# Kernel optimization log

Hardware: AMD Instinct MI355X
Metric: run time of the kernel (lower is better)

The kernel has to match this reference:

```python
import jax, jax.numpy as jnp
import numpy as np

K = 3
STRIDE = 1
PAD = 1
DIL = 1


def _conv2d(x, w, b, stride, pad):
    y = jax.lax.conv_general_dilated(
        x, w, (stride, stride), [(pad, pad), (pad, pad)],
        dimension_numbers=('NCHW', 'OIHW', 'NCHW'))
    return y + b[None, :, None, None]


def setup_inputs() -> dict:
    key = jax.random.key(0)
    ks = jax.random.split(key, 6)
    N, Cin, Cout, H, W = 4, 64, 64, 128, 128
    x = jax.random.normal(ks[0], (N, Cin, H, W), jnp.float32)
    w_off = jax.random.normal(ks[1], (2 * K * K, Cin, K, K), jnp.float32) * 0.01
    b_off = jnp.zeros((2 * K * K,), jnp.float32)
    w_mask = jax.random.normal(ks[2], (K * K, Cin, K, K), jnp.float32) * 0.01
    b_mask = jnp.zeros((K * K,), jnp.float32)
    weight = jax.random.normal(ks[3], (Cout, Cin, K, K), jnp.float32) * 0.05
    bias = jax.random.normal(ks[4], (Cout,), jnp.float32)
    return {"x": x, "w_off": w_off, "b_off": b_off,
            "w_mask": w_mask, "b_mask": b_mask,
            "weight": weight, "bias": bias}


def _deform_conv(x, offset, weight, bias):
    # x: [N,C,H,W]; offset: [N,2*K2,Ho,Wo] with channel layout (dy,dx) per kernel pt
    N, C, H, W = x.shape
    K2 = K * K
    Ho, Wo = offset.shape[2], offset.shape[3]
    off_y = offset[:, 0::2]  # [N,K2,Ho,Wo]
    off_x = offset[:, 1::2]
    ki = jnp.arange(K2) // K
    kj = jnp.arange(K2) % K
    base_y = (jnp.arange(Ho) * STRIDE - PAD)[None, :, None] + (ki * DIL)[:, None, None]
    base_x = (jnp.arange(Wo) * STRIDE - PAD)[None, None, :] + (kj * DIL)[:, None, None]
    py = base_y[None].astype(off_y.dtype) + off_y  # [N,K2,Ho,Wo]
    px = base_x[None].astype(off_x.dtype) + off_x
    y0 = jnp.floor(py)
    x0 = jnp.floor(px)
    wy = py - y0
    wx = px - x0
    xf = x.reshape(N, C, H * W)

    def corner(yi, xi):
        valid = (yi >= 0) & (yi <= H - 1) & (xi >= 0) & (xi <= W - 1)
        yc = jnp.clip(yi, 0, H - 1).astype(jnp.int32)
        xc = jnp.clip(xi, 0, W - 1).astype(jnp.int32)
        idx = (yc * W + xc).reshape(N, -1)  # [N, K2*Ho*Wo]
        g = jnp.take_along_axis(xf, idx[:, None, :], axis=2)  # [N,C,K2*Ho*Wo]
        g = g.reshape(N, C, K2, Ho, Wo)
        return g * valid[:, None].astype(x.dtype)

    # bilinear interpolation with zero padding outside the image
    val = ((1 - wy) * (1 - wx))[:, None] * corner(y0, x0) \
        + ((1 - wy) * wx)[:, None] * corner(y0, x0 + 1) \
        + (wy * (1 - wx))[:, None] * corner(y0 + 1, x0) \
        + (wy * wx)[:, None] * corner(y0 + 1, x0 + 1)  # [N,C,K2,Ho,Wo]
    out = jnp.einsum('nckhw,ock->nohw', val,
                     weight.reshape(weight.shape[0], C, K2))
    return out + bias[None, :, None, None]


def reference(x, w_off, b_off, w_mask, b_mask, weight, bias):
    offset = _conv2d(x, w_off, b_off, STRIDE, PAD)              # [N,2*K2,Ho,Wo]
    mask = jax.nn.sigmoid(_conv2d(x, w_mask, b_mask, STRIDE, PAD))  # [N,K2,Ho,Wo]
    # source does mask.repeat(1,2,1,1) then offset*mask, then plain deform_conv2d
    offset = offset * jnp.concatenate([mask, mask], axis=1)
    return _deform_conv(x, offset, weight, bias)
```

## Files before the change

### kernel.cpp

```cpp
#include <hip/hip_runtime.h>
#include <math.h>

#define HD 128
#define WD 128
#define WP 130
#define CIN 64
#define COUT 64
#define NB 4
#define K2 9
#define HW (HD*WD)
#define CK 576
#define TP 32
#define TPF 16
#define NKK 18

#define WAM   (4 * NKK * 64 * 8)
#define WAO   (2 * NKK * 64 * 8)
#define XTP   ((size_t)NB * WP * WP * CIN)
#define OFFSZ ((size_t)NB * K2 * HW)
#define WTSZ  ((size_t)CK * COUT)

#define PRE_T 1024
#define PRE_H 65
#define PRE_P ((WAM + WAO) / 256)
#define HALO_PER_N 33024
#define HALO_W8 16512

typedef __attribute__((ext_vector_type(8))) short short8;
typedef __attribute__((ext_vector_type(4))) float f32x4;

__device__ inline unsigned short f2bf(float v) {
    unsigned int u = __float_as_uint(v);
    unsigned int r = u + 0x7fffu + ((u >> 16) & 1u);
    return (unsigned short)(r >> 16);
}
__device__ inline float bf2f(unsigned short b) {
    return __uint_as_float(((unsigned int)b) << 16);
}
__device__ inline unsigned int pack_bf16(float a, float b) {
#if __has_builtin(__builtin_amdgcn_cvt_pk_bf16_f32)
    auto r = __builtin_amdgcn_cvt_pk_bf16_f32(a, b);
    unsigned int u; __builtin_memcpy(&u, &r, 4); return u;
#else
    return ((unsigned int)f2bf(b) << 16) | (unsigned int)f2bf(a);
#endif
}
__device__ inline float2 up2(unsigned int u) {
    float2 r;
    r.x = __uint_as_float(u << 16);
    r.y = __uint_as_float(u & 0xffff0000u);
    return r;
}

__global__ __launch_bounds__(256) void pre_kernel(
    const float* __restrict__ x,
    const float* __restrict__ weight,
    const float* __restrict__ w_off,
    const float* __restrict__ w_mask,
    unsigned short* __restrict__ xp,
    short* __restrict__ mhi, short* __restrict__ ohi)
{
    __shared__ float tile[64][66];
    int bid = blockIdx.x;
    int t = threadIdx.x;

    if (bid < PRE_T) {
        int half = bid & 1;
        int h = (bid >> 1) & 127;
        int n = bid >> 8;
        int w0 = half * 64;
        int g = t >> 6, wl = t & 63;
        const float* xb = x + ((size_t)n * CIN) * HW + h * WD + w0;
        #pragma unroll
        for (int i = 0; i < 16; i++) {
            int cc = i * 4 + g;
            tile[wl][cc] = xb[(size_t)cc * HW + wl];
        }
        __syncthreads();
        size_t rowbase = (((size_t)n * WP + (h + 1)) * WP + (w0 + 1)) * CIN;
        #pragma unroll
        for (int i = 0; i < 8; i++) {
            int u = i * 256 + t;
            int ww = u >> 5;
            int cp = (u & 31) * 2;
            float2 v = *(const float2*)&tile[ww][cp];
            *(unsigned int*)&xp[rowbase + (size_t)ww * CIN + cp] = pack_bf16(v.x, v.y);
        }
    } else if (bid < PRE_T + PRE_H) {
        int widx = (bid - PRE_T) * 256 + t;
        if (widx < HALO_W8) {
            int s = widx * 8;
            int n = s / HALO_PER_N;
            int v = s - n * HALO_PER_N;
            size_t nb = (size_t)n * WP * WP * CIN;
            size_t base;
            if (v < 8320) {
                base = nb + v;
            } else if (v < 16640) {
                base = nb + (size_t)129 * WP * CIN + (v - 8320);
            } else if (v < 24832) {
                int v2 = v - 16640; int h = 1 + (v2 >> 6); int c = v2 & 63;
                base = nb + (size_t)h * WP * CIN + c;
            } else {
                int v3 = v - 24832; int h = 1 + (v3 >> 6); int c = v3 & 63;
                base = nb + ((size_t)h * WP + 129) * CIN + c;
            }
            short8 z = {0, 0, 0, 0, 0, 0, 0, 0};
            *(short8*)&xp[base] = z;
        }
    } else {
        int gid = (bid - PRE_T - PRE_H) * 256 + t;
        if (gid < WAM) {
            int idx = gid;
            int jj = idx & 7;
            int lane = (idx >> 3) & 63;
            int kk = (idx >> 9) % NKK;
            int mt = (idx >> 9) / NKK;
            int o = mt * 16 + (lane & 15);
            int rp = kk * 32 + (lane >> 4) * 8 + jj;
            int k = rp >> 6, c = rp & 63;
            mhi[idx] = (short)f2bf(weight[((size_t)o * CIN + c) * 9 + k]);
        } else {
            int idx = gid - WAM;
            int jj = idx & 7;
            int lane = (idx >> 3) & 63;
            int kk = (idx >> 9) % NKK;
            int mt = (idx >> 9) / NKK;
            int j = mt * 16 + (lane & 15);
            int rp = kk * 32 + (lane >> 4) * 8 + jj;
            int k = rp >> 6, c = rp & 63;
            float w = 0.f;
            if (j < 18)      w = w_off[((size_t)j * CIN + c) * 9 + k];
            else if (j < 27) w = w_mask[((size_t)(j - 18) * CIN + c) * 9 + k];
            ohi[idx] = (short)f2bf(w);
        }
    }
}

__global__ __launch_bounds__(256, 4) void fused_kernel(
    const unsigned short* __restrict__ xp,
    const short* __restrict__ waM_hi,
    const short* __restrict__ waO_hi,
    const float* __restrict__ b_off, const float* __restrict__ b_mask,
    const float* __restrict__ bias,
    float* __restrict__ out)
{
    __shared__ __align__(16) short val_s[72 * 256];
    __shared__ __align__(16) float U[27 * 32];

    int t = threadIdx.x;
    int wv = t >> 6;
    int lane = t & 63;
    int wo0 = blockIdx.x * TP;
    int ho  = blockIdx.y;
    int n   = blockIdx.z;
    const unsigned short* xpn = xp + (size_t)n * WP * WP * CIN;
    int p16 = lane & 15, quad = lane >> 4;

    #pragma unroll
    for (int i = 0; i < 9; i++) {
        int u = t + 256 * i;
        int tap = u >> 8;
        int p = (u >> 3) & 31;
        int g = u & 7;
        int ti = tap / 3, tj = tap - ti * 3;
        const short8 v = *(const short8*)&xpn[((size_t)(ho + ti) * WP + (wo0 + p + tj)) * CIN + g * 8];
        int c2 = tap * 8 + g;
        *(short8*)&val_s[c2 * 256 + ((p + c2) & 31) * 8] = v;
    }
    __syncthreads();

    {
        int jt = wv >> 1, pt = wv & 1;
        f32x4 acc = {0.f, 0.f, 0.f, 0.f};
        #pragma unroll
        for (int kk = 0; kk < NKK; kk++) {
            int abase = ((jt * NKK + kk) * 64 + lane) * 8;
            short8 ah = *(const short8*)&waO_hi[abase];
            int c2 = kk * 4 + quad;
            short8 b = *(const short8*)&val_s[c2 * 256 + ((pt * 16 + p16 + c2) & 31) * 8];
            acc = __builtin_amdgcn_mfma_f32_16x16x32_bf16(ah, b, acc, 0, 0, 0);
        }
        #pragma unroll
        for (int i = 0; i < 4; i++) {
            int j = jt * 16 + quad * 4 + i;
            if (j < 27) {
                float bv = (j < 18) ? b_off[j] : b_mask[j - 18];
                U[j * 32 + pt * 16 + p16] = acc[i] + bv;
            }
        }
    }
    __syncthreads();

    float rwy[2], rwx[2];
    unsigned int rmeta[2];
    #pragma unroll
    for (int pass = 0; pass < 2; pass++) {
        int u = t + pass * 256;
        if (u < K2 * TP) {
            int k = u >> 5, p = u & 31;
            float oy_raw = U[(2 * k) * 32 + p];
            float ox_raw = U[(2 * k + 1) * 32 + p];
            float my = 1.f / (1.f + expf(-U[(18 + (2 * k) % 9) * 32 + p]));
            float mx = 1.f / (1.f + expf(-U[(18 + (2 * k + 1) % 9) * 32 + p]));
            float oy = oy_raw * my;
            float ox = ox_raw * mx;
            int ki = k / 3, kj = k - ki * 3;
            int wo = wo0 + p;
            float py = (float)(ho - 1 + ki) + oy;
            float px = (float)(wo - 1 + kj) + ox;
            float y0f = floorf(py), x0f = floorf(px);
            float wy = py - y0f, wx = px - x0f;
            int y0 = (int)y0f, x0 = (int)x0f;
            int y0c = min(max(y0, 0), HD - 1);
            int y1c = min(max(y0 + 1, 0), HD - 1);
            int x0c = min(max(x0, 0), WD - 1);
            int x1c = min(max(x0 + 1, 0), WD - 1);
            bool vy0 = (y0 >= 0) && (y0 < HD);
            bool vy1 = (y0 + 1 >= 0) && (y0 + 1 < HD);
            bool vx0 = (x0 >= 0) && (x0 < WD);
            bool vx1 = (x0 + 1 >= 0) && (x0 + 1 < WD);
            unsigned int cvA = (vy0 && vx0) ? 1u : 0u;
            unsigned int cvB = (vy0 && vx1) ? 1u : 0u;
            unsigned int cvC = (vy1 && vx0) ? 1u : 0u;
            unsigned int cvD = (vy1 && vx1) ? 1u : 0u;
            rwy[pass] = wy;
            rwx[pass] = wx;
            rmeta[pass] = (unsigned int)y0c | ((unsigned int)x0c << 7)
                        | ((unsigned int)(y1c - y0c) << 14) | ((unsigned int)(x1c - x0c) << 15)
                        | (cvA << 16) | (cvB << 17) | (cvC << 18) | (cvD << 19);
        }
    }
    __syncthreads();
    #pragma unroll
    for (int pass = 0; pass < 2; pass++) {
        int u = t + pass * 256;
        if (u < K2 * TP) {
            U[u] = rwy[pass];
            U[288 + u] = rwx[pass];
            ((unsigned int*)U)[576 + u] = rmeta[pass];
        }
    }
    __syncthreads();

    #pragma unroll
    for (int i = 0; i < 9; i++) {
        int u = t + 256 * i;
        int task = u >> 3;
        int g = u & 7;
        int c0 = g * 8;
        int k = task >> 5, p = task & 31;
        float wy = U[task];
        float wx = U[288 + task];
        unsigned int m = ((const unsigned int*)U)[576 + task];
        float wy0 = 1.f - wy, wx0 = 1.f - wx;
        float wA = (m & 0x10000u) ? wy0 * wx0 : 0.f;
        float wB = (m & 0x20000u) ? wy0 * wx  : 0.f;
        float wC = (m & 0x40000u) ? wy  * wx0 : 0.f;
        float wD = (m & 0x80000u) ? wy  * wx  : 0.f;
        int y0c = (int)(m & 127u);
        int x0c = (int)((m >> 7) & 127u);
        int ry0 = (y0c + 1) * (WP * CIN);
        int ry1 = ry0 + (int)((m >> 14) & 1u) * (WP * CIN);
        int cx0 = (x0c + 1) * CIN;
        int cx1 = cx0 + (int)((m >> 15) & 1u) * CIN;
        int ia = ry0 + cx0 + c0;
        int ib = ry0 + cx1 + c0;
        int ic = ry1 + cx0 + c0;
        int id = ry1 + cx1 + c0;
        uint4 qa = *(const uint4*)&xpn[ia];
        uint4 qb = *(const uint4*)&xpn[ib];
        uint4 qc = *(const uint4*)&xpn[ic];
        uint4 qd = *(const uint4*)&xpn[id];
        unsigned int qa_[4] = {qa.x, qa.y, qa.z, qa.w};
        unsigned int qb_[4] = {qb.x, qb.y, qb.z, qb.w};
        unsigned int qc_[4] = {qc.x, qc.y, qc.z, qc.w};
        unsigned int qd_[4] = {qd.x, qd.y, qd.z, qd.w};
        unsigned int r_[4];
        #pragma unroll
        for (int d = 0; d < 4; d++) {
            float2 fa = up2(qa_[d]), fb = up2(qb_[d]), fc = up2(qc_[d]), fd = up2(qd_[d]);
            float2 gg;
            gg.x = wA * fa.x + wB * fb.x + wC * fc.x + wD * fd.x;
            gg.y = wA * fa.y + wB * fb.y + wC * fc.y + wD * fd.y;
            r_[d] = pack_bf16(gg.x, gg.y);
        }
        uint4 r = {r_[0], r_[1], r_[2], r_[3]};
        int c2 = k * 8 + g;
        *(uint4*)&val_s[c2 * 256 + ((p + c2) & 31) * 8] = r;
    }
    __syncthreads();

    f32x4 a0 = {0.f, 0.f, 0.f, 0.f};
    f32x4 a1 = {0.f, 0.f, 0.f, 0.f};
    #pragma unroll
    for (int kk = 0; kk < NKK; kk++) {
        int abase = ((wv * NKK + kk) * 64 + lane) * 8;
        short8 ah = *(const short8*)&waM_hi[abase];
        int c2 = kk * 4 + quad;
        short8 b0 = *(const short8*)&val_s[c2 * 256 + ((p16 + c2) & 31) * 8];
        short8 b1 = *(const short8*)&val_s[c2 * 256 + ((16 + p16 + c2) & 31) * 8];
        a0 = __builtin_amdgcn_mfma_f32_16x16x32_bf16(ah, b0, a0, 0, 0, 0);
        a1 = __builtin_amdgcn_mfma_f32_16x16x32_bf16(ah, b1, a1, 0, 0, 0);
    }

    size_t obase = ((size_t)n * COUT) * HW + (size_t)ho * WD + wo0;
    #pragma unroll
    for (int i = 0; i < 4; i++) {
        int o = wv * 16 + quad * 4 + i;
        float bv = bias[o];
        out[obase + (size_t)o * HW + p16] = a0[i] + bv;
        out[obase + (size_t)o * HW + 16 + p16] = a1[i] + bv;
    }
}

__global__ void transpose_w_kernel(const float* __restrict__ w, float* __restrict__ wt) {
    int i = blockIdx.x * 256 + threadIdx.x;
    int o = i / CK;
    int ck = i - o * CK;
    wt[ck * COUT + o] = w[i];
}

__global__ __launch_bounds__(256) void offmask_kernel(
    const float* __restrict__ x,
    const float* __restrict__ w_off, const float* __restrict__ b_off,
    const float* __restrict__ w_mask, const float* __restrict__ b_mask,
    float* __restrict__ offy, float* __restrict__ offx)
{
    __shared__ float ws[CK][27];
    int t = threadIdx.x;
    for (int i = t; i < CK * 27; i += 256) {
        int j = i % 27;
        int citap = i / 27;
        int ci = citap / 9;
        int tap = citap - ci * 9;
        float v;
        if (j < 18) v = w_off[(j * CIN + ci) * 9 + tap];
        else        v = w_mask[((j - 18) * CIN + ci) * 9 + tap];
        ws[citap][j] = v;
    }
    __syncthreads();

    int pix = blockIdx.x * 256 + t;
    int n  = pix >> 14;
    int ho = (pix >> 7) & 127;
    int wo = pix & 127;

    float acc[27];
    #pragma unroll
    for (int j = 0; j < 18; j++) acc[j] = b_off[j];
    #pragma unroll
    for (int j = 0; j < 9; j++)  acc[18 + j] = b_mask[j];

    int offs[9];
    bool oks[9];
    #pragma unroll
    for (int dy = 0; dy < 3; dy++) {
        int y = ho - 1 + dy;
        #pragma unroll
        for (int dx = 0; dx < 3; dx++) {
            int xx = wo - 1 + dx;
            bool ok = (y >= 0) && (y < HD) && (xx >= 0) && (xx < WD);
            oks[dy * 3 + dx] = ok;
            offs[dy * 3 + dx] = (ok ? y : 0) * WD + (ok ? xx : 0);
        }
    }
    const float* xn = x + (size_t)n * CIN * HW;
    for (int ci = 0; ci < CIN; ci++) {
        const float* xc = xn + (size_t)ci * HW;
        float v[9];
        #pragma unroll
        for (int tap = 0; tap < 9; tap++)
            v[tap] = oks[tap] ? xc[offs[tap]] : 0.f;
        #pragma unroll
        for (int tap = 0; tap < 9; tap++) {
            const float* wrow = ws[ci * 9 + tap];
            float vv = v[tap];
            #pragma unroll
            for (int j = 0; j < 27; j++) acc[j] += wrow[j] * vv;
        }
    }
    float m[9];
    #pragma unroll
    for (int j = 0; j < 9; j++) m[j] = 1.f / (1.f + expf(-acc[18 + j]));
    #pragma unroll
    for (int k = 0; k < 9; k++) {
        int cy = 2 * k, cx = 2 * k + 1;
        float my = m[cy < 9 ? cy : cy - 9];
        float mx = m[cx < 9 ? cx : cx - 9];
        size_t o = (((size_t)n * K2 + k) * HD + ho) * WD + wo;
        offy[o] = acc[cy] * my;
        offx[o] = acc[cx] * mx;
    }
}

__global__ __launch_bounds__(256) void deform_kernel(
    const float* __restrict__ x,
    const float* __restrict__ offy, const float* __restrict__ offx,
    const float* __restrict__ wt,
    const float* __restrict__ bias,
    float* __restrict__ out)
{
    __shared__ __align__(16) float val_f[CK * TPF];
    __shared__ float4 p_w4[K2 * TPF];
    __shared__ int4   p_idx4[K2 * TPF];

    int t = threadIdx.x;
    int wo0 = blockIdx.x * TPF;
    int ho  = blockIdx.y;
    int n   = blockIdx.z;

    if (t < K2 * TPF) {
        int k = t >> 4, p = t & 15;
        int wo = wo0 + p;
        size_t oi = (((size_t)n * K2 + k) * HD + ho) * WD + wo;
        float oy = offy[oi], ox = offx[oi];
        int ki = k / 3, kj = k - ki * 3;
        float py = (float)(ho - 1 + ki) + oy;
        float px = (float)(wo - 1 + kj) + ox;
        float y0f = floorf(py), x0f = floorf(px);
        float wy = py - y0f, wx = px - x0f;
        int y0 = (int)y0f, x0 = (int)x0f;
        float wy0 = 1.f - wy, wx0 = 1.f - wx;
        int y0c = min(max(y0, 0), HD - 1);
        int y1c = min(max(y0 + 1, 0), HD - 1);
        int x0c = min(max(x0, 0), WD - 1);
        int x1c = min(max(x0 + 1, 0), WD - 1);
        bool vy0 = (y0 >= 0) && (y0 < HD);
        bool vy1 = (y0 + 1 >= 0) && (y0 + 1 < HD);
        bool vx0 = (x0 >= 0) && (x0 < WD);
        bool vx1 = (x0 + 1 >= 0) && (x0 + 1 < WD);
        float4 w4;
        w4.x = (vy0 && vx0) ? wy0 * wx0 : 0.f;
        w4.y = (vy0 && vx1) ? wy0 * wx  : 0.f;
        w4.z = (vy1 && vx0) ? wy  * wx0 : 0.f;
        w4.w = (vy1 && vx1) ? wy  * wx  : 0.f;
        int4 i4;
        i4.x = y0c * WD + x0c;
        i4.y = y0c * WD + x1c;
        i4.z = y1c * WD + x0c;
        i4.w = y1c * WD + x1c;
        p_w4[t] = w4;
        p_idx4[t] = i4;
    }
    __syncthreads();

    const float* xn = x + (size_t)n * CIN * HW;
    for (int e = t; e < CK * TPF; e += 256) {
        int row = e >> 4, p = e & 15;
        int cc = row / 9, k = row - cc * 9;
        int task = (k << 4) | p;
        float4 w4 = p_w4[task];
        int4  i4 = p_idx4[task];
        const float* xc = xn + (size_t)cc * HW;
        val_f[e] = w4.x * xc[i4.x] + w4.y * xc[i4.y]
                 + w4.z * xc[i4.z] + w4.w * xc[i4.w];
    }
    __syncthreads();

    int o = t & 63, q = t >> 6;
    float4 acc = {0.f, 0.f, 0.f, 0.f};
    const float4* v4 = (const float4*)val_f;
    const float* wp = wt + o;
    #pragma unroll 4
    for (int r = 0; r < CK; r++) {
        float w = wp[r * COUT];
        float4 vv = v4[r * 4 + q];
        acc.x += w * vv.x; acc.y += w * vv.y;
        acc.z += w * vv.z; acc.w += w * vv.w;
    }
    float b = bias[o];
    acc.x += b; acc.y += b; acc.z += b; acc.w += b;
    __syncthreads();
    float4* o4 = (float4*)val_f;
    o4[o * 4 + q] = acc;
    __syncthreads();
    size_t obase = ((size_t)n * COUT) * HW + (size_t)ho * WD + wo0;
    #pragma unroll
    for (int i = 0; i < 4; i++) {
        int l = t + 256 * i;
        int oo = l >> 4, p = l & 15;
        out[obase + (size_t)oo * HW + p] = val_f[l];
    }
}

extern "C" void kernel_launch(void* const* d_in, const int* in_sizes, int n_in,
                              void* d_out, int out_size, void* d_ws, size_t ws_size,
                              hipStream_t stream) {
    const float* x      = (const float*)d_in[0];
    const float* w_off  = (const float*)d_in[1];
    const float* b_off  = (const float*)d_in[2];
    const float* w_mask = (const float*)d_in[3];
    const float* b_mask = (const float*)d_in[4];
    const float* weight = (const float*)d_in[5];
    const float* bias   = (const float*)d_in[6];
    float* out = (float*)d_out;

    short* base = (short*)d_ws;
    short* waM_hi = base;
    short* waO_hi = waM_hi + WAM;
    unsigned short* xp = (unsigned short*)(waO_hi + WAO);
    size_t need = ((size_t)WAM + WAO + XTP) * sizeof(short);

    if (ws_size >= need) {
        pre_kernel<<<PRE_T + PRE_H + PRE_P, 256, 0, stream>>>(
            x, weight, w_off, w_mask, xp, waM_hi, waO_hi);
        fused_kernel<<<dim3(WD / TP, HD, NB), 256, 0, stream>>>(
            xp, waM_hi, waO_hi, b_off, b_mask, bias, out);
    } else {
        float* offy = (float*)d_ws;
        float* offx = offy + OFFSZ;
        float* wt   = offx + OFFSZ;
        transpose_w_kernel<<<144, 256, 0, stream>>>(weight, wt);
        offmask_kernel<<<256, 256, 0, stream>>>(x, w_off, b_off, w_mask, b_mask, offy, offx);
        deform_kernel<<<dim3(WD / TPF, HD, NB), 256, 0, stream>>>(x, offy, offx, wt, bias, out);
    }
}
```

Before: 111.3 us.

## Fuse offset setup into bilinear sampling with software-pipelined corner gathers

Drops the separate pass that computed per-tap bilinear metadata into shared memory, along with its two barriers. Each thread now handles one pixel and channel group across all 9 taps, computing the 9 sigmoid masks once and prefetching corner loads two taps ahead in a 3-slot register ring. The im2col staging loop is also restructured so all 9 global loads are issued before the shared stores. The cost is redundant offset math (each of the 8 channel-group threads recomputes it) and higher register pressure, which could hurt occupancy under launch_bounds(256,4).

```diff
diff --git a/kernel.cpp b/kernel.cpp
--- a/kernel.cpp
+++ b/kernel.cpp
@@ -137,6 +137,37 @@
     }
 }
 
+#define TAP_SETUP(kc, s) { \
+    const int kk_ = (kc); \
+    float oy = U[(2 * kk_) * 32 + p] * msk[(2 * kk_) % 9]; \
+    float ox = U[(2 * kk_ + 1) * 32 + p] * msk[(2 * kk_ + 1) % 9]; \
+    const int ki_ = kk_ / 3, kj_ = kk_ - ki_ * 3; \
+    float py = (float)(ho - 1 + ki_) + oy; \
+    float px = (float)(wo0 + p - 1 + kj_) + ox; \
+    float y0f = floorf(py), x0f = floorf(px); \
+    float wy = py - y0f, wx = px - x0f; \
+    int y0 = (int)y0f, x0 = (int)x0f; \
+    int y0c = min(max(y0, 0), HD - 1); \
+    int y1c = min(max(y0 + 1, 0), HD - 1); \
+    int x0c = min(max(x0, 0), WD - 1); \
+    int x1c = min(max(x0 + 1, 0), WD - 1); \
+    bool vy0 = (y0 >= 0) && (y0 < HD); \
+    bool vy1 = (y0 + 1 >= 0) && (y0 + 1 < HD); \
+    bool vx0 = (x0 >= 0) && (x0 < WD); \
+    bool vx1 = (x0 + 1 >= 0) && (x0 + 1 < WD); \
+    float wy0 = 1.f - wy, wx0 = 1.f - wx; \
+    wAv[s] = (vy0 && vx0) ? wy0 * wx0 : 0.f; \
+    wBv[s] = (vy0 && vx1) ? wy0 * wx  : 0.f; \
+    wCv[s] = (vy1 && vx0) ? wy  * wx0 : 0.f; \
+    wDv[s] = (vy1 && vx1) ? wy  * wx  : 0.f; \
+    int ry0 = (y0c + 1) * (WP * CIN), ry1 = (y1c + 1) * (WP * CIN); \
+    int cx0 = (x0c + 1) * CIN + c0, cx1 = (x1c + 1) * CIN + c0; \
+    qav[s] = *(const uint4*)&xpn[ry0 + cx0]; \
+    qbv[s] = *(const uint4*)&xpn[ry0 + cx1]; \
+    qcv[s] = *(const uint4*)&xpn[ry1 + cx0]; \
+    qdv[s] = *(const uint4*)&xpn[ry1 + cx1]; \
+}
+
 __global__ __launch_bounds__(256, 4) void fused_kernel(
     const unsigned short* __restrict__ xp,
     const short* __restrict__ waM_hi,
@@ -157,16 +188,19 @@
     const unsigned short* xpn = xp + (size_t)n * WP * WP * CIN;
     int p16 = lane & 15, quad = lane >> 4;
 
-    #pragma unroll
-    for (int i = 0; i < 9; i++) {
-        int u = t + 256 * i;
-        int tap = u >> 8;
-        int p = (u >> 3) & 31;
-        int g = u & 7;
-        int ti = tap / 3, tj = tap - ti * 3;
-        const short8 v = *(const short8*)&xpn[((size_t)(ho + ti) * WP + (wo0 + p + tj)) * CIN + g * 8];
-        int c2 = tap * 8 + g;
-        *(short8*)&val_s[c2 * 256 + ((p + c2) & 31) * 8] = v;
+    {
+        int p = t >> 3, g = t & 7;
+        short8 s1[9];
+        #pragma unroll
+        for (int i = 0; i < 9; i++) {
+            int ti = i / 3, tj = i - ti * 3;
+            s1[i] = *(const short8*)&xpn[((size_t)(ho + ti) * WP + (wo0 + p + tj)) * CIN + g * 8];
+        }
+        #pragma unroll
+        for (int i = 0; i < 9; i++) {
+            int c2 = i * 8 + g;
+            *(short8*)&val_s[c2 * 256 + ((p + c2) & 31) * 8] = s1[i];
+        }
     }
     __syncthreads();
 
@@ -192,102 +226,38 @@
     }
     __syncthreads();
 
-    float rwy[2], rwx[2];
-    unsigned int rmeta[2];
-    #pragma unroll
-    for (int pass = 0; pass < 2; pass++) {
-        int u = t + pass * 256;
-        if (u < K2 * TP) {
-            int k = u >> 5, p = u & 31;
-            float oy_raw = U[(2 * k) * 32 + p];
-            float ox_raw = U[(2 * k + 1) * 32 + p];
-            float my = 1.f / (1.f + expf(-U[(18 + (2 * k) % 9) * 32 + p]));
-            float mx = 1.f / (1.f + expf(-U[(18 + (2 * k + 1) % 9) * 32 + p]));
-            float oy = oy_raw * my;
-            float ox = ox_raw * mx;
-            int ki = k / 3, kj = k - ki * 3;
-            int wo = wo0 + p;
-            float py = (float)(ho - 1 + ki) + oy;
-            float px = (float)(wo - 1 + kj) + ox;
-            float y0f = floorf(py), x0f = floorf(px);
-            float wy = py - y0f, wx = px - x0f;
-            int y0 = (int)y0f, x0 = (int)x0f;
-            int y0c = min(max(y0, 0), HD - 1);
-            int y1c = min(max(y0 + 1, 0), HD - 1);
-            int x0c = min(max(x0, 0), WD - 1);
-            int x1c = min(max(x0 + 1, 0), WD - 1);
-            bool vy0 = (y0 >= 0) && (y0 < HD);
-            bool vy1 = (y0 + 1 >= 0) && (y0 + 1 < HD);
-            bool vx0 = (x0 >= 0) && (x0 < WD);
-            bool vx1 = (x0 + 1 >= 0) && (x0 + 1 < WD);
-            unsigned int cvA = (vy0 && vx0) ? 1u : 0u;
-            unsigned int cvB = (vy0 && vx1) ? 1u : 0u;
-            unsigned int cvC = (vy1 && vx0) ? 1u : 0u;
-            unsigned int cvD = (vy1 && vx1) ? 1u : 0u;
-            rwy[pass] = wy;
-            rwx[pass] = wx;
-            rmeta[pass] = (unsigned int)y0c | ((unsigned int)x0c << 7)
-                        | ((unsigned int)(y1c - y0c) << 14) | ((unsigned int)(x1c - x0c) << 15)
-                        | (cvA << 16) | (cvB << 17) | (cvC << 18) | (cvD << 19);
-        }
-    }
-    __syncthreads();
-    #pragma unroll
-    for (int pass = 0; pass < 2; pass++) {
-        int u = t + pass * 256;
-        if (u < K2 * TP) {
-            U[u] = rwy[pass];
-            U[288 + u] = rwx[pass];
-            ((unsigned int*)U)[576 + u] = rmeta[pass];
-        }
-    }
-    __syncthreads();
-
-    #pragma unroll
-    for (int i = 0; i < 9; i++) {
-        int u = t + 256 * i;
-        int task = u >> 3;
-        int g = u & 7;
-        int c0 = g * 8;
-        int k = task >> 5, p = task & 31;
-        float wy = U[task];
-        float wx = U[288 + task];
-        unsigned int m = ((const unsigned int*)U)[576 + task];
-        float wy0 = 1.f - wy, wx0 = 1.f - wx;
-        float wA = (m & 0x10000u) ? wy0 * wx0 : 0.f;
-        float wB = (m & 0x20000u) ? wy0 * wx  : 0.f;
-        float wC = (m & 0x40000u) ? wy  * wx0 : 0.f;
-        float wD = (m & 0x80000u) ? wy  * wx  : 0.f;
-        int y0c = (int)(m & 127u);
-        int x0c = (int)((m >> 7) & 127u);
-        int ry0 = (y0c + 1) * (WP * CIN);
-        int ry1 = ry0 + (int)((m >> 14) & 1u) * (WP * CIN);
-        int cx0 = (x0c + 1) * CIN;
-        int cx1 = cx0 + (int)((m >> 15) & 1u) * CIN;
-        int ia = ry0 + cx0 + c0;
-        int ib = ry0 + cx1 + c0;
-        int ic = ry1 + cx0 + c0;
-        int id = ry1 + cx1 + c0;
-        uint4 qa = *(const uint4*)&xpn[ia];
-        uint4 qb = *(const uint4*)&xpn[ib];
-        uint4 qc = *(const uint4*)&xpn[ic];
-        uint4 qd = *(const uint4*)&xpn[id];
-        unsigned int qa_[4] = {qa.x, qa.y, qa.z, qa.w};
-        unsigned int qb_[4] = {qb.x, qb.y, qb.z, qb.w};
-        unsigned int qc_[4] = {qc.x, qc.y, qc.z, qc.w};
-        unsigned int qd_[4] = {qd.x, qd.y, qd.z, qd.w};
-        unsigned int r_[4];
-        #pragma unroll
-        for (int d = 0; d < 4; d++) {
-            float2 fa = up2(qa_[d]), fb = up2(qb_[d]), fc = up2(qc_[d]), fd = up2(qd_[d]);
-            float2 gg;
-            gg.x = wA * fa.x + wB * fb.x + wC * fc.x + wD * fd.x;
-            gg.y = wA * fa.y + wB * fb.y + wC * fc.y + wD * fd.y;
-            r_[d] = pack_bf16(gg.x, gg.y);
-        }
-        uint4 r = {r_[0], r_[1], r_[2], r_[3]};
-        int c2 = k * 8 + g;
-        *(uint4*)&val_s[c2 * 256 + ((p + c2) & 31) * 8] = r;
+    {
+        int p = t >> 3, g = t & 7, c0 = g * 8;
+        float msk[9];
+        #pragma unroll
+        for (int j = 0; j < 9; j++)
+            msk[j] = 1.f / (1.f + expf(-U[(18 + j) * 32 + p]));
+
+        float wAv[3], wBv[3], wCv[3], wDv[3];
+        uint4 qav[3], qbv[3], qcv[3], qdv[3];
+        TAP_SETUP(0, 0);
+        TAP_SETUP(1, 1);
+        #pragma unroll
+        for (int k = 0; k < 9; k++) {
+            if (k < 7) TAP_SETUP(k + 2, (k + 2) % 3);
+            const int s = k % 3;
+            unsigned int qa_[4] = {qav[s].x, qav[s].y, qav[s].z, qav[s].w};
+            unsigned int qb_[4] = {qbv[s].x, qbv[s].y, qbv[s].z, qbv[s].w};
+            unsigned int qc_[4] = {qcv[s].x, qcv[s].y, qcv[s].z, qcv[s].w};
+            unsigned int qd_[4] = {qdv[s].x, qdv[s].y, qdv[s].z, qdv[s].w};
+            unsigned int r_[4];
+            #pragma unroll
+            for (int d = 0; d < 4; d++) {
+                float2 fa = up2(qa_[d]), fb = up2(qb_[d]), fc = up2(qc_[d]), fd = up2(qd_[d]);
+                float2 gg;
+                gg.x = wAv[s] * fa.x + wBv[s] * fb.x + wCv[s] * fc.x + wDv[s] * fd.x;
+                gg.y = wAv[s] * fa.y + wBv[s] * fb.y + wCv[s] * fc.y + wDv[s] * fd.y;
+                r_[d] = pack_bf16(gg.x, gg.y);
+            }
+            uint4 r = {r_[0], r_[1], r_[2], r_[3]};
+            int c2 = k * 8 + g;
+            *(uint4*)&val_s[c2 * 256 + ((p + c2) & 31) * 8] = r;
+        }
     }
     __syncthreads();
 
```

New measurement: 113.8 us. +2.3%, slower.
